# Kernel optimization log

Hardware: AMD Instinct MI355X
Metric: run time of the kernel (lower is better)

## Reference

```python
import jax, jax.numpy as jnp
import numpy as np

N = 100000      # n_nodes
D = 64          # in_features == out_features (elementwise W mul requires equality)
DEG = 16        # avg degree for random edges
H = 2           # n_head
ALPHA = 0.2     # LeakyReLU negative slope


def setup_inputs() -> dict:
    key = jax.random.key(0)
    k1, k2, k3 = jax.random.split(key, 3)
    inputs = jax.random.normal(k1, (N, D), dtype=jnp.float32)
    # random edges + self-loops so every row has at least one edge (nonzero rowsum)
    rnd = jax.random.randint(k2, (2, N * DEG), 0, N)
    self_loops = jnp.tile(jnp.arange(N)[None, :], (2, 1))
    edge_index = jnp.concatenate([self_loops, rnd], axis=1)  # [2, 1.7M]
    # per-head params, matching torch init: W = ones, a ~ U(-stdv, stdv)
    W = jnp.ones((H, D), dtype=jnp.float32)
    stdv = 1.0 / np.sqrt(D * 2)
    a = jax.random.uniform(k3, (H, 2 * D), dtype=jnp.float32, minval=-stdv, maxval=stdv)
    return {"inputs": inputs, "edge_index": edge_index, "W": W, "a": a}


def reference(inputs, edge_index, W, a):
    n = inputs.shape[0]
    row, col = edge_index[0], edge_index[1]

    def head(Wh, ah):
        h = inputs * Wh  # [N, D]
        # a @ [h_src; h_dst] decomposes into per-node dots, then scalar edge gather
        score = (h @ ah[:D])[row] + (h @ ah[D:])[col]          # [E]
        e = jnp.exp(jnp.where(score > 0, score, ALPHA * score))  # exp(leaky_relu)
        rowsum = jax.ops.segment_sum(e, row, num_segments=n)     # [N]
        # sparse.mm(coo(edge, e), inputs): h_prime[i] = sum_j e_ij * inputs[j]
        h_prime = jax.ops.segment_sum(e[:, None] * inputs[col], row, num_segments=n)
        return h_prime / rowsum[:, None]

    outs = jax.vmap(head)(W, a)  # [H, N, D]
    return outs.mean(axis=0)
```

## Files before the change

kernel.cpp:

```cpp
#include <hip/hip_runtime.h>


#define D 64
#define ALPHA 0.2f
#define CAP 96
#define BSHIFT 9
#define BROWS 512
#define MAXBUK 256
#define TILE 2048
#define PACKSHIFT 23
#define COLMASK ((1u << PACKSHIFT) - 1u)

__device__ __forceinline__ unsigned bf16rne(float f) {
    unsigned u = __float_as_uint(f);
    u += 0x7fffu + ((u >> 16) & 1u);
    return u >> 16;
}
__device__ __forceinline__ float lrexp(float sc) {
    return __expf(sc > 0.f ? sc : ALPHA * sc);
}

__global__ __launch_bounds__(256) void k_front(
    const float* __restrict__ x, const float* __restrict__ W,
    const float* __restrict__ a, float4* __restrict__ s,
    unsigned short* __restrict__ xh, const int* __restrict__ row,
    unsigned short* __restrict__ tcnt, int N, int E, int nblkA)
{
    __shared__ int h[MAXBUK];
    if ((int)blockIdx.x < nblkA) {
        int wid  = (blockIdx.x * 256 + threadIdx.x) >> 6;
        int lane = threadIdx.x & 63;
        if (wid >= N) return;
        float v = x[(size_t)wid * D + lane];
        xh[(size_t)wid * D + lane] = (unsigned short)bf16rne(v);
        float h0 = v * W[lane];
        float h1 = v * W[D + lane];
        float t0 = h0 * a[lane];
        float t1 = h0 * a[D + lane];
        float t2 = h1 * a[2 * D + lane];
        float t3 = h1 * a[3 * D + lane];
#pragma unroll
        for (int off = 32; off; off >>= 1) {
            t0 += __shfl_xor(t0, off);
            t1 += __shfl_xor(t1, off);
            t2 += __shfl_xor(t2, off);
            t3 += __shfl_xor(t3, off);
        }
        if (lane == 0) s[wid] = make_float4(t0, t1, t2, t3);
    } else {
        int tile = blockIdx.x - nblkA;
        int t = threadIdx.x, base = tile * TILE;
        int cnt = E - base; if (cnt > TILE) cnt = TILE;
        h[t] = 0;
        __syncthreads();
        for (int i = t; i < cnt; i += 256) atomicAdd(&h[row[base + i] >> BSHIFT], 1);
        __syncthreads();
        tcnt[(size_t)tile * MAXBUK + t] = (unsigned short)h[t];
    }
}

__global__ __launch_bounds__(256) void k_col_scan(
    const unsigned short* __restrict__ tcnt, int* __restrict__ tbase,
    int* __restrict__ bcnt, int NT)
{
    __shared__ int wsum[256];
    int b = blockIdx.x, t = threadIdx.x;
    int t4 = t * 4;
    int v0 = (t4     < NT) ? tcnt[(size_t)(t4    ) * MAXBUK + b] : 0;
    int v1 = (t4 + 1 < NT) ? tcnt[(size_t)(t4 + 1) * MAXBUK + b] : 0;
    int v2 = (t4 + 2 < NT) ? tcnt[(size_t)(t4 + 2) * MAXBUK + b] : 0;
    int v3 = (t4 + 3 < NT) ? tcnt[(size_t)(t4 + 3) * MAXBUK + b] : 0;
    int sv = v0 + v1 + v2 + v3;
    wsum[t] = sv;
    __syncthreads();
    for (int off = 1; off < 256; off <<= 1) {
        int add = (t >= off) ? wsum[t - off] : 0;
        __syncthreads();
        wsum[t] += add;
        __syncthreads();
    }
    int run = wsum[t] - sv;
    if (t4     < NT) { tbase[(size_t)(t4    ) * MAXBUK + b] = run; run += v0; }
    if (t4 + 1 < NT) { tbase[(size_t)(t4 + 1) * MAXBUK + b] = run; run += v1; }
    if (t4 + 2 < NT) { tbase[(size_t)(t4 + 2) * MAXBUK + b] = run; run += v2; }
    if (t4 + 3 < NT) { tbase[(size_t)(t4 + 3) * MAXBUK + b] = run; run += v3; }
    if (t == 255) bcnt[b] = wsum[255];
}

__global__ void k_bucket_scan(const int* __restrict__ bcnt,
                              int* __restrict__ bbase, int nbuk)
{
    __shared__ int sd[MAXBUK];
    int t = threadIdx.x;
    int v = (t < nbuk) ? bcnt[t] : 0;
    sd[t] = v;
    __syncthreads();
    for (int off = 1; off < MAXBUK; off <<= 1) {
        int add = (t >= off) ? sd[t - off] : 0;
        __syncthreads();
        sd[t] += add;
        __syncthreads();
    }
    if (t < nbuk) bbase[t] = sd[t] - v;
    if (t == nbuk - 1) bbase[nbuk] = sd[t];
}

__global__ __launch_bounds__(256) void k_binning(
    const int* __restrict__ row, const int* __restrict__ col,
    const unsigned short* __restrict__ tcnt, const int* __restrict__ bbase,
    const int* __restrict__ tbase, unsigned* __restrict__ ebuf, int E)
{
    __shared__ int lrow[TILE];
    __shared__ int lcol[TILE];
    __shared__ int st[MAXBUK];
    __shared__ int gb[MAXBUK];
    __shared__ int cur[MAXBUK];
    __shared__ int wsum[256];
    int t = threadIdx.x;
    int tile = blockIdx.x;
    int base = tile * TILE;
    int cnt = E - base; if (cnt > TILE) cnt = TILE;

    int h = tcnt[(size_t)tile * MAXBUK + t];
    wsum[t] = h;
    __syncthreads();
    for (int off = 1; off < 256; off <<= 1) {
        int add = (t >= off) ? wsum[t - off] : 0;
        __syncthreads();
        wsum[t] += add;
        __syncthreads();
    }
    int start = wsum[t] - h;
    st[t]  = start;
    cur[t] = start;
    gb[t]  = bbase[t] + tbase[(size_t)tile * MAXBUK + t];
    __syncthreads();

    for (int i = t; i < cnt; i += 256) {
        int r = row[base + i], c = col[base + i];
        int p = atomicAdd(&cur[r >> BSHIFT], 1);
        lrow[p] = r; lcol[p] = c;
    }
    __syncthreads();

    for (int i = t; i < cnt; i += 256) {
        int rr = lrow[i];
        int bb = rr >> BSHIFT;
        ebuf[gb[bb] + (i - st[bb])] =
            ((unsigned)(rr & (BROWS - 1)) << PACKSHIFT) | (unsigned)lcol[i];
    }
}

__global__ __launch_bounds__(1024) void k_rowsort(
    const unsigned* __restrict__ ebuf, const int* __restrict__ bbase,
    int* __restrict__ offsets, int* __restrict__ counts,
    int* __restrict__ scol, int N)
{
    __shared__ int hist[BROWS];
    __shared__ int offs[BROWS];
    __shared__ int wsum[256];
    int b = blockIdx.x, t = threadIdx.x;
    int lo = b << BSHIFT;
    int s0 = bbase[b], s1 = bbase[b + 1];

    if (t < BROWS) hist[t] = 0;
    __syncthreads();
    for (int i = s0 + t; i < s1; i += 1024)
        atomicAdd(&hist[ebuf[i] >> PACKSHIFT], 1);
    __syncthreads();

    int a0 = 0, a1 = 0, sv = 0;
    if (t < 256) { a0 = hist[2 * t]; a1 = hist[2 * t + 1]; sv = a0 + a1; wsum[t] = sv; }
    __syncthreads();
    for (int off = 1; off < 256; off <<= 1) {
        int add = 0;
        if (t < 256 && t >= off) add = wsum[t - off];
        __syncthreads();
        if (t < 256) wsum[t] += add;
        __syncthreads();
    }
    if (t < 256) { int run = wsum[t] - sv; offs[2 * t] = run; offs[2 * t + 1] = run + a0; }
    __syncthreads();

    if (t < BROWS) {
        int rg = lo + t;
        if (rg < N) { offsets[rg] = s0 + offs[t]; counts[rg] = hist[t]; }
    }
    __syncthreads();
    if (t < BROWS) hist[t] = offs[t];
    __syncthreads();

    for (int i = s0 + t; i < s1; i += 1024) {
        unsigned pk = ebuf[i];
        int p = atomicAdd(&hist[pk >> PACKSHIFT], 1);
        scol[s0 + p] = (int)(pk & COLMASK);
    }
}

__global__ __launch_bounds__(256) void k_gather(
    const unsigned* __restrict__ xh2, const float4* __restrict__ s,
    const int* __restrict__ offsets, const int* __restrict__ counts,
    const int* __restrict__ scol, float* __restrict__ out, int N)
{
    __shared__ float  le0[4][CAP];
    __shared__ float  le1[4][CAP];
    __shared__ float2 lpair[4][CAP];
    int w    = threadIdx.x >> 6;
    int lane = threadIdx.x & 63;
    int n    = blockIdx.x * 4 + w;
    bool valid = (n < N);
    int start = 0, cnt = 0;
    float4 srow = make_float4(0.f, 0.f, 0.f, 0.f);
    if (valid) { start = offsets[n]; cnt = counts[n]; srow = s[n]; }

    float sum0 = 0.f, sum1 = 0.f;
    for (int k = lane; k < cnt; k += 64) {
        int c = scol[start + k];
        float4 sc = s[c];
        float e0 = lrexp(srow.x + sc.y);
        float e1 = lrexp(srow.z + sc.w);
        sum0 += e0; sum1 += e1;
        if (k < CAP) { lpair[w][k].x = __int_as_float(c << 5); le0[w][k] = e0; le1[w][k] = e1; }
    }
    int m  = cnt < CAP ? cnt : CAP;
    int mp = (m + 7) & ~7;
    {
        int k = m + lane;
        if (k < mp) { lpair[w][k].x = __int_as_float(0); le0[w][k] = 0.f; le1[w][k] = 0.f; }
    }
#pragma unroll
    for (int off = 32; off; off >>= 1) {
        sum0 += __shfl_xor(sum0, off);
        sum1 += __shfl_xor(sum1, off);
    }
    if (!valid) return;
    float inv0 = 0.5f / sum0, inv1 = 0.5f / sum1;
    for (int k = lane; k < mp; k += 64)
        lpair[w][k].y = inv0 * le0[w][k] + inv1 * le1[w][k];

    int q  = lane >> 4;
    int li = lane & 15;
    float a0 = 0.f, a1 = 0.f, a2 = 0.f, a3 = 0.f;
    for (int k = 0; k < mp; k += 8) {
#pragma unroll
        for (int j = 0; j < 2; j++) {
            int kk = k + 4 * j + q;
            float2 pr = lpair[w][kk];
            unsigned cb = (unsigned)__float_as_int(pr.x);
            uint2 u = *(const uint2*)(xh2 + cb + 2 * li);
            float cf = pr.y;
            a0 += cf * __uint_as_float(u.x << 16);
            a1 += cf * __uint_as_float(u.x & 0xffff0000u);
            a2 += cf * __uint_as_float(u.y << 16);
            a3 += cf * __uint_as_float(u.y & 0xffff0000u);
        }
    }
    for (int kk = CAP + q; kk < cnt; kk += 4) {
        int c = scol[start + kk];
        float4 sc = s[c];
        float cf = inv0 * lrexp(srow.x + sc.y) + inv1 * lrexp(srow.z + sc.w);
        uint2 u = *(const uint2*)(xh2 + ((unsigned)c << 5) + 2 * li);
        a0 += cf * __uint_as_float(u.x << 16);
        a1 += cf * __uint_as_float(u.x & 0xffff0000u);
        a2 += cf * __uint_as_float(u.y << 16);
        a3 += cf * __uint_as_float(u.y & 0xffff0000u);
    }
    a0 += __shfl_xor(a0, 16); a0 += __shfl_xor(a0, 32);
    a1 += __shfl_xor(a1, 16); a1 += __shfl_xor(a1, 32);
    a2 += __shfl_xor(a2, 16); a2 += __shfl_xor(a2, 32);
    a3 += __shfl_xor(a3, 16); a3 += __shfl_xor(a3, 32);
    if (q == 0)
        ((float4*)(out + (size_t)n * D))[li] = make_float4(a0, a1, a2, a3);
}

extern "C" void kernel_launch(void* const* d_in, const int* in_sizes, int n_in,
                              void* d_out, int out_size, void* d_ws, size_t ws_size,
                              hipStream_t stream)
{
    const float* x  = (const float*)d_in[0];
    const int*   ei = (const int*)d_in[1];
    const float* W  = (const float*)d_in[2];
    const float* a  = (const float*)d_in[3];
    float*       out = (float*)d_out;
    int N = in_sizes[0] / D;
    int E = in_sizes[1] / 2;
    const int* row = ei;
    const int* col = ei + E;

    int NBUK = (N + BROWS - 1) >> BSHIFT;
    int NT   = (E + TILE - 1) / TILE;

    uintptr_t wp = (uintptr_t)d_ws;
    auto alloc = [&wp](size_t bytes) -> void* {
        wp = (wp + 255) & ~(uintptr_t)255;
        void* p = (void*)wp;
        wp += bytes;
        return p;
    };
    unsigned short* xh      = (unsigned short*)alloc((size_t)N * D * 2);
    float4*         s       = (float4*)alloc((size_t)N * sizeof(float4));
    int*            offsets = (int*)alloc((size_t)N * sizeof(int));
    int*            counts  = (int*)alloc((size_t)N * sizeof(int));
    int*            scol    = (int*)alloc((size_t)E * sizeof(int));
    unsigned*       ebuf    = (unsigned*)alloc((size_t)E * sizeof(unsigned));
    int*            tbase   = (int*)alloc((size_t)NT * MAXBUK * sizeof(int));
    int*            bcnt    = (int*)alloc(MAXBUK * sizeof(int));
    int*            bbase   = (int*)alloc((MAXBUK + 4) * sizeof(int));
    unsigned short* tcnt    = (unsigned short*)alloc((size_t)NT * MAXBUK * 2);

    int nblkA = (N + 3) / 4;
    k_front<<<nblkA + NT, 256, 0, stream>>>(x, W, a, s, xh, row, tcnt, N, E, nblkA);
    k_col_scan<<<NBUK, 256, 0, stream>>>(tcnt, tbase, bcnt, NT);
    k_bucket_scan<<<1, MAXBUK, 0, stream>>>(bcnt, bbase, NBUK);
    k_binning<<<NT, 256, 0, stream>>>(row, col, tcnt, bbase, tbase, ebuf, E);
    k_rowsort<<<NBUK, 1024, 0, stream>>>(ebuf, bbase, offsets, counts, scol, N);
    k_gather<<<(N + 3) / 4, 256, 0, stream>>>((const unsigned*)xh, s, offsets, counts, scol, out, N);
}
```

Measured before the change: 188.3 us.

## Compute softmax coefficients in row-sort and stream precomputed fp16 weights in gather

Moves per-edge exp(leaky_relu) scoring and row normalisation out of the gather kernel into the row-sort kernel. That kernel now uses 256-row buckets, stages edges in shared memory, and writes pre-shifted column offsets plus fp16 combined coefficients, so the gather becomes a plain weighted sum. It also folds the bucket scan into the binning kernel, removing one launch, and vectorises the front kernel to float4 with four nodes per wave. The trade-offs are extra fp16 rounding of attention weights, larger shared-memory use in row-sort, and a slow fallback path for oversized buckets.

```diff
diff --git a/kernel.cpp b/kernel.cpp
--- a/kernel.cpp
+++ b/kernel.cpp
@@ -1,15 +1,16 @@
 #include <hip/hip_runtime.h>
+#include <hip/hip_fp16.h>
 
 
 #define D 64
 #define ALPHA 0.2f
-#define CAP 96
-#define BSHIFT 9
-#define BROWS 512
-#define MAXBUK 256
+#define BSHIFT 8
+#define BROWS 256
+#define MAXBUK 512
 #define TILE 2048
-#define PACKSHIFT 23
-#define COLMASK ((1u << PACKSHIFT) - 1u)
+#define PK2 17
+#define M17 ((1u << PK2) - 1u)
+#define CAPE 6144
 
 __device__ __forceinline__ unsigned bf16rne(float f) {
     unsigned u = __float_as_uint(f);
@@ -19,52 +20,71 @@
 __device__ __forceinline__ float lrexp(float sc) {
     return __expf(sc > 0.f ? sc : ALPHA * sc);
 }
+__device__ __forceinline__ unsigned packe(float e0, float e1) {
+    __half2 h = __floats2half2_rn(e0, e1);
+    return *reinterpret_cast<unsigned*>(&h);
+}
+__device__ __forceinline__ float2 unpacke(unsigned u) {
+    __half2 h = *reinterpret_cast<__half2*>(&u);
+    return __half22float2(h);
+}
 
 __global__ __launch_bounds__(256) void k_front(
     const float* __restrict__ x, const float* __restrict__ W,
     const float* __restrict__ a, float4* __restrict__ s,
-    unsigned short* __restrict__ xh, const int* __restrict__ row,
+    unsigned* __restrict__ xh2, const int* __restrict__ row,
     unsigned short* __restrict__ tcnt, int N, int E, int nblkA)
 {
     __shared__ int h[MAXBUK];
     if ((int)blockIdx.x < nblkA) {
         int wid  = (blockIdx.x * 256 + threadIdx.x) >> 6;
         int lane = threadIdx.x & 63;
-        if (wid >= N) return;
-        float v = x[(size_t)wid * D + lane];
-        xh[(size_t)wid * D + lane] = (unsigned short)bf16rne(v);
-        float h0 = v * W[lane];
-        float h1 = v * W[D + lane];
-        float t0 = h0 * a[lane];
-        float t1 = h0 * a[D + lane];
-        float t2 = h1 * a[2 * D + lane];
-        float t3 = h1 * a[3 * D + lane];
+        int node = wid * 4 + (lane >> 4);
+        int f4   = lane & 15;
+        if (node >= N) return;
+        const float4* x4 = (const float4*)x;
+        const float4* W4 = (const float4*)W;
+        const float4* A4 = (const float4*)a;
+        float4 v  = x4[(size_t)node * 16 + f4];
+        unsigned u01 = (bf16rne(v.y) << 16) | bf16rne(v.x);
+        unsigned u23 = (bf16rne(v.w) << 16) | bf16rne(v.z);
+        *(uint2*)(xh2 + (size_t)node * 32 + 2 * f4) = make_uint2(u01, u23);
+        float4 w0 = W4[f4], w1 = W4[16 + f4];
+        float4 a0 = A4[f4], a1 = A4[16 + f4], a2 = A4[32 + f4], a3 = A4[48 + f4];
+        float4 h0 = make_float4(v.x * w0.x, v.y * w0.y, v.z * w0.z, v.w * w0.w);
+        float4 h1 = make_float4(v.x * w1.x, v.y * w1.y, v.z * w1.z, v.w * w1.w);
+        float t0 = h0.x * a0.x + h0.y * a0.y + h0.z * a0.z + h0.w * a0.w;
+        float t1 = h0.x * a1.x + h0.y * a1.y + h0.z * a1.z + h0.w * a1.w;
+        float t2 = h1.x * a2.x + h1.y * a2.y + h1.z * a2.z + h1.w * a2.w;
+        float t3 = h1.x * a3.x + h1.y * a3.y + h1.z * a3.z + h1.w * a3.w;
 #pragma unroll
-        for (int off = 32; off; off >>= 1) {
+        for (int off = 1; off < 16; off <<= 1) {
             t0 += __shfl_xor(t0, off);
             t1 += __shfl_xor(t1, off);
             t2 += __shfl_xor(t2, off);
             t3 += __shfl_xor(t3, off);
         }
-        if (lane == 0) s[wid] = make_float4(t0, t1, t2, t3);
+        if (f4 == 0) s[node] = make_float4(t0, t1, t2, t3);
     } else {
         int tile = blockIdx.x - nblkA;
         int t = threadIdx.x, base = tile * TILE;
         int cnt = E - base; if (cnt > TILE) cnt = TILE;
-        h[t] = 0;
+        h[t] = 0; h[t + 256] = 0;
         __syncthreads();
         for (int i = t; i < cnt; i += 256) atomicAdd(&h[row[base + i] >> BSHIFT], 1);
         __syncthreads();
-        tcnt[(size_t)tile * MAXBUK + t] = (unsigned short)h[t];
+        tcnt[(size_t)tile * MAXBUK + t]       = (unsigned short)h[t];
+        tcnt[(size_t)tile * MAXBUK + t + 256] = (unsigned short)h[t + 256];
     }
 }
 
 __global__ __launch_bounds__(256) void k_col_scan(
     const unsigned short* __restrict__ tcnt, int* __restrict__ tbase,
-    int* __restrict__ bcnt, int NT)
-{
+    int* __restrict__ bcnt, int NT, int nbuk)
+{
+    int b = blockIdx.x, t = threadIdx.x;
+    if (b >= nbuk) { if (t == 0) bcnt[b] = 0; return; }
     __shared__ int wsum[256];
-    int b = blockIdx.x, t = threadIdx.x;
     int t4 = t * 4;
     int v0 = (t4     < NT) ? tcnt[(size_t)(t4    ) * MAXBUK + b] : 0;
     int v1 = (t4 + 1 < NT) ? tcnt[(size_t)(t4 + 1) * MAXBUK + b] : 0;
@@ -87,53 +107,56 @@
     if (t == 255) bcnt[b] = wsum[255];
 }
 
-__global__ void k_bucket_scan(const int* __restrict__ bcnt,
-                              int* __restrict__ bbase, int nbuk)
-{
-    __shared__ int sd[MAXBUK];
-    int t = threadIdx.x;
-    int v = (t < nbuk) ? bcnt[t] : 0;
-    sd[t] = v;
-    __syncthreads();
-    for (int off = 1; off < MAXBUK; off <<= 1) {
-        int add = (t >= off) ? sd[t - off] : 0;
-        __syncthreads();
-        sd[t] += add;
-        __syncthreads();
-    }
-    if (t < nbuk) bbase[t] = sd[t] - v;
-    if (t == nbuk - 1) bbase[nbuk] = sd[t];
-}
-
 __global__ __launch_bounds__(256) void k_binning(
     const int* __restrict__ row, const int* __restrict__ col,
-    const unsigned short* __restrict__ tcnt, const int* __restrict__ bbase,
-    const int* __restrict__ tbase, unsigned* __restrict__ ebuf, int E)
+    const unsigned short* __restrict__ tcnt, const int* __restrict__ bcnt,
+    const int* __restrict__ tbase, unsigned* __restrict__ ebuf,
+    int* __restrict__ bbase_g, int E)
 {
     __shared__ int lrow[TILE];
     __shared__ int lcol[TILE];
     __shared__ int st[MAXBUK];
     __shared__ int gb[MAXBUK];
     __shared__ int cur[MAXBUK];
-    __shared__ int wsum[256];
+    __shared__ int w2[256];
     int t = threadIdx.x;
     int tile = blockIdx.x;
     int base = tile * TILE;
     int cnt = E - base; if (cnt > TILE) cnt = TILE;
 
-    int h = tcnt[(size_t)tile * MAXBUK + t];
-    wsum[t] = h;
+    int h0 = tcnt[(size_t)tile * MAXBUK + 2 * t];
+    int h1 = tcnt[(size_t)tile * MAXBUK + 2 * t + 1];
+    int sv = h0 + h1;
+    w2[t] = sv;
     __syncthreads();
     for (int off = 1; off < 256; off <<= 1) {
-        int add = (t >= off) ? wsum[t - off] : 0;
-        __syncthreads();
-        wsum[t] += add;
-        __syncthreads();
-    }
-    int start = wsum[t] - h;
-    st[t]  = start;
-    cur[t] = start;
-    gb[t]  = bbase[t] + tbase[(size_t)tile * MAXBUK + t];
+        int add = (t >= off) ? w2[t - off] : 0;
+        __syncthreads();
+        w2[t] += add;
+        __syncthreads();
+    }
+    int run = w2[t] - sv;
+    st[2 * t] = run;       st[2 * t + 1] = run + h0;
+    cur[2 * t] = run;      cur[2 * t + 1] = run + h0;
+    __syncthreads();
+
+    int b0 = bcnt[2 * t], b1 = bcnt[2 * t + 1];
+    int sb = b0 + b1;
+    w2[t] = sb;
+    __syncthreads();
+    for (int off = 1; off < 256; off <<= 1) {
+        int add = (t >= off) ? w2[t - off] : 0;
+        __syncthreads();
+        w2[t] += add;
+        __syncthreads();
+    }
+    int runb = w2[t] - sb;
+    gb[2 * t]     = runb      + tbase[(size_t)tile * MAXBUK + 2 * t];
+    gb[2 * t + 1] = runb + b0 + tbase[(size_t)tile * MAXBUK + 2 * t + 1];
+    if (tile == 0) {
+        bbase_g[2 * t] = runb; bbase_g[2 * t + 1] = runb + b0;
+        if (t == 255) bbase_g[512] = runb + b0 + b1;
+    }
     __syncthreads();
 
     for (int i = t; i < cnt; i += 256) {
@@ -147,119 +170,126 @@
         int rr = lrow[i];
         int bb = rr >> BSHIFT;
         ebuf[gb[bb] + (i - st[bb])] =
-            ((unsigned)(rr & (BROWS - 1)) << PACKSHIFT) | (unsigned)lcol[i];
+            ((unsigned)(rr & (BROWS - 1)) << PK2) | (unsigned)lcol[i];
     }
 }
 
 __global__ __launch_bounds__(1024) void k_rowsort(
     const unsigned* __restrict__ ebuf, const int* __restrict__ bbase,
-    int* __restrict__ offsets, int* __restrict__ counts,
-    int* __restrict__ scol, int N)
-{
-    __shared__ int hist[BROWS];
-    __shared__ int offs[BROWS];
-    __shared__ int wsum[256];
+    const float4* __restrict__ s, int* __restrict__ offsets,
+    int* __restrict__ counts, unsigned* __restrict__ scol,
+    __half* __restrict__ ecoef, int N)
+{
+    __shared__ unsigned lpk[CAPE];
+    __shared__ unsigned lev[CAPE];
+    __shared__ int   hist[BROWS];
+    __shared__ int   offs[BROWS];
+    __shared__ int   cursor[BROWS];
+    __shared__ float rs0[BROWS], rs1[BROWS];
+    __shared__ float rsx[BROWS], rsz[BROWS];
+    __shared__ int   wsum[256];
     int b = blockIdx.x, t = threadIdx.x;
     int lo = b << BSHIFT;
     int s0 = bbase[b], s1 = bbase[b + 1];
-
-    if (t < BROWS) hist[t] = 0;
-    __syncthreads();
+    int seg = s1 - s0;
+
+    if (t < BROWS) {
+        int g = lo + t;
+        float4 f = (g < N) ? s[g] : make_float4(0.f, 0.f, 0.f, 0.f);
+        rsx[t] = f.x; rsz[t] = f.z;
+        hist[t] = 0; rs0[t] = 0.f; rs1[t] = 0.f;
+    }
+    __syncthreads();
+
     for (int i = s0 + t; i < s1; i += 1024)
-        atomicAdd(&hist[ebuf[i] >> PACKSHIFT], 1);
-    __syncthreads();
-
-    int a0 = 0, a1 = 0, sv = 0;
-    if (t < 256) { a0 = hist[2 * t]; a1 = hist[2 * t + 1]; sv = a0 + a1; wsum[t] = sv; }
+        atomicAdd(&hist[ebuf[i] >> PK2], 1);
+    __syncthreads();
+
+    int a = 0;
+    if (t < BROWS) { a = hist[t]; wsum[t] = a; }
     __syncthreads();
     for (int off = 1; off < 256; off <<= 1) {
         int add = 0;
-        if (t < 256 && t >= off) add = wsum[t - off];
-        __syncthreads();
-        if (t < 256) wsum[t] += add;
-        __syncthreads();
-    }
-    if (t < 256) { int run = wsum[t] - sv; offs[2 * t] = run; offs[2 * t + 1] = run + a0; }
-    __syncthreads();
-
-    if (t < BROWS) {
-        int rg = lo + t;
-        if (rg < N) { offsets[rg] = s0 + offs[t]; counts[rg] = hist[t]; }
-    }
-    __syncthreads();
-    if (t < BROWS) hist[t] = offs[t];
-    __syncthreads();
-
-    for (int i = s0 + t; i < s1; i += 1024) {
-        unsigned pk = ebuf[i];
-        int p = atomicAdd(&hist[pk >> PACKSHIFT], 1);
-        scol[s0 + p] = (int)(pk & COLMASK);
+        if (t < BROWS && t >= off) add = wsum[t - off];
+        __syncthreads();
+        if (t < BROWS) wsum[t] += add;
+        __syncthreads();
+    }
+    if (t < BROWS) { offs[t] = wsum[t] - a; cursor[t] = wsum[t] - a; }
+    __syncthreads();
+
+    if (seg <= CAPE) {
+        for (int i = s0 + t; i < s1; i += 1024) {
+            unsigned pk = ebuf[i];
+            int r = pk >> PK2, c = (int)(pk & M17);
+            float4 sc = s[c];
+            float e0 = lrexp(rsx[r] + sc.y);
+            float e1 = lrexp(rsz[r] + sc.w);
+            atomicAdd(&rs0[r], e0);
+            atomicAdd(&rs1[r], e1);
+            int p = atomicAdd(&cursor[r], 1);
+            lpk[p] = pk; lev[p] = packe(e0, e1);
+        }
+        __syncthreads();
+        if (t < BROWS) {
+            rs0[t] = 0.5f / rs0[t]; rs1[t] = 0.5f / rs1[t];
+            int rg = lo + t;
+            if (rg < N) { offsets[rg] = s0 + offs[t]; counts[rg] = hist[t]; }
+        }
+        __syncthreads();
+        for (int i = t; i < seg; i += 1024) {
+            unsigned pk = lpk[i];
+            int r = pk >> PK2;
+            float2 ef = unpacke(lev[i]);
+            float coef = rs0[r] * ef.x + rs1[r] * ef.y;
+            scol[s0 + i]  = (pk & M17) << 5;
+            ecoef[s0 + i] = __float2half(coef);
+        }
+    } else {
+        for (int i = s0 + t; i < s1; i += 1024) {
+            unsigned pk = ebuf[i];
+            int r = pk >> PK2, c = (int)(pk & M17);
+            float4 sc = s[c];
+            atomicAdd(&rs0[r], lrexp(rsx[r] + sc.y));
+            atomicAdd(&rs1[r], lrexp(rsz[r] + sc.w));
+        }
+        __syncthreads();
+        if (t < BROWS) {
+            rs0[t] = 0.5f / rs0[t]; rs1[t] = 0.5f / rs1[t];
+            int rg = lo + t;
+            if (rg < N) { offsets[rg] = s0 + offs[t]; counts[rg] = hist[t]; }
+        }
+        __syncthreads();
+        for (int i = s0 + t; i < s1; i += 1024) {
+            unsigned pk = ebuf[i];
+            int r = pk >> PK2, c = (int)(pk & M17);
+            float4 sc = s[c];
+            float coef = rs0[r] * lrexp(rsx[r] + sc.y)
+                       + rs1[r] * lrexp(rsz[r] + sc.w);
+            int p = atomicAdd(&cursor[r], 1);
+            scol[s0 + p]  = (unsigned)c << 5;
+            ecoef[s0 + p] = __float2half(coef);
+        }
     }
 }
 
 __global__ __launch_bounds__(256) void k_gather(
-    const unsigned* __restrict__ xh2, const float4* __restrict__ s,
-    const int* __restrict__ offsets, const int* __restrict__ counts,
-    const int* __restrict__ scol, float* __restrict__ out, int N)
-{
-    __shared__ float  le0[4][CAP];
-    __shared__ float  le1[4][CAP];
-    __shared__ float2 lpair[4][CAP];
+    const unsigned* __restrict__ xh2, const int* __restrict__ offsets,
+    const int* __restrict__ counts, const unsigned* __restrict__ scol,
+    const __half* __restrict__ ecoef, float* __restrict__ out, int N)
+{
     int w    = threadIdx.x >> 6;
     int lane = threadIdx.x & 63;
     int n    = blockIdx.x * 4 + w;
-    bool valid = (n < N);
-    int start = 0, cnt = 0;
-    float4 srow = make_float4(0.f, 0.f, 0.f, 0.f);
-    if (valid) { start = offsets[n]; cnt = counts[n]; srow = s[n]; }
-
-    float sum0 = 0.f, sum1 = 0.f;
-    for (int k = lane; k < cnt; k += 64) {
-        int c = scol[start + k];
-        float4 sc = s[c];
-        float e0 = lrexp(srow.x + sc.y);
-        float e1 = lrexp(srow.z + sc.w);
-        sum0 += e0; sum1 += e1;
-        if (k < CAP) { lpair[w][k].x = __int_as_float(c << 5); le0[w][k] = e0; le1[w][k] = e1; }
-    }
-    int m  = cnt < CAP ? cnt : CAP;
-    int mp = (m + 7) & ~7;
-    {
-        int k = m + lane;
-        if (k < mp) { lpair[w][k].x = __int_as_float(0); le0[w][k] = 0.f; le1[w][k] = 0.f; }
-    }
-#pragma unroll
-    for (int off = 32; off; off >>= 1) {
-        sum0 += __shfl_xor(sum0, off);
-        sum1 += __shfl_xor(sum1, off);
-    }
-    if (!valid) return;
-    float inv0 = 0.5f / sum0, inv1 = 0.5f / sum1;
-    for (int k = lane; k < mp; k += 64)
-        lpair[w][k].y = inv0 * le0[w][k] + inv1 * le1[w][k];
-
+    if (n >= N) return;
+    int start = offsets[n], cnt = counts[n];
     int q  = lane >> 4;
     int li = lane & 15;
     float a0 = 0.f, a1 = 0.f, a2 = 0.f, a3 = 0.f;
-    for (int k = 0; k < mp; k += 8) {
-#pragma unroll
-        for (int j = 0; j < 2; j++) {
-            int kk = k + 4 * j + q;
-            float2 pr = lpair[w][kk];
-            unsigned cb = (unsigned)__float_as_int(pr.x);
-            uint2 u = *(const uint2*)(xh2 + cb + 2 * li);
-            float cf = pr.y;
-            a0 += cf * __uint_as_float(u.x << 16);
-            a1 += cf * __uint_as_float(u.x & 0xffff0000u);
-            a2 += cf * __uint_as_float(u.y << 16);
-            a3 += cf * __uint_as_float(u.y & 0xffff0000u);
-        }
-    }
-    for (int kk = CAP + q; kk < cnt; kk += 4) {
-        int c = scol[start + kk];
-        float4 sc = s[c];
-        float cf = inv0 * lrexp(srow.x + sc.y) + inv1 * lrexp(srow.z + sc.w);
-        uint2 u = *(const uint2*)(xh2 + ((unsigned)c << 5) + 2 * li);
+    for (int kk = q; kk < cnt; kk += 4) {
+        unsigned cb = scol[start + kk];
+        float cf = __half2float(ecoef[start + kk]);
+        uint2 u = *(const uint2*)(xh2 + cb + 2 * li);
         a0 += cf * __uint_as_float(u.x << 16);
         a1 += cf * __uint_as_float(u.x & 0xffff0000u);
         a2 += cf * __uint_as_float(u.y << 16);
@@ -297,22 +327,22 @@
         wp += bytes;
         return p;
     };
-    unsigned short* xh      = (unsigned short*)alloc((size_t)N * D * 2);
+    unsigned*       xh2     = (unsigned*)alloc((size_t)N * 32 * 4);
     float4*         s       = (float4*)alloc((size_t)N * sizeof(float4));
     int*            offsets = (int*)alloc((size_t)N * sizeof(int));
     int*            counts  = (int*)alloc((size_t)N * sizeof(int));
-    int*            scol    = (int*)alloc((size_t)E * sizeof(int));
+    unsigned*       scol    = (unsigned*)alloc((size_t)E * sizeof(unsigned));
     unsigned*       ebuf    = (unsigned*)alloc((size_t)E * sizeof(unsigned));
+    __half*         ecoef   = (__half*)alloc((size_t)E * sizeof(__half));
     int*            tbase   = (int*)alloc((size_t)NT * MAXBUK * sizeof(int));
     int*            bcnt    = (int*)alloc(MAXBUK * sizeof(int));
     int*            bbase   = (int*)alloc((MAXBUK + 4) * sizeof(int));
     unsigned short* tcnt    = (unsigned short*)alloc((size_t)NT * MAXBUK * 2);
 
-    int nblkA = (N + 3) / 4;
-    k_front<<<nblkA + NT, 256, 0, stream>>>(x, W, a, s, xh, row, tcnt, N, E, nblkA);
-    k_col_scan<<<NBUK, 256, 0, stream>>>(tcnt, tbase, bcnt, NT);
-    k_bucket_scan<<<1, MAXBUK, 0, stream>>>(bcnt, bbase, NBUK);
-    k_binning<<<NT, 256, 0, stream>>>(row, col, tcnt, bbase, tbase, ebuf, E);
-    k_rowsort<<<NBUK, 1024, 0, stream>>>(ebuf, bbase, offsets, counts, scol, N);
-    k_gather<<<(N + 3) / 4, 256, 0, stream>>>((const unsigned*)xh, s, offsets, counts, scol, out, N);
-}
+    int nblkA = (N + 15) / 16;
+    k_front<<<nblkA + NT, 256, 0, stream>>>(x, W, a, s, xh2, row, tcnt, N, E, nblkA);
+    k_col_scan<<<MAXBUK, 256, 0, stream>>>(tcnt, tbase, bcnt, NT, NBUK);
+    k_binning<<<NT, 256, 0, stream>>>(row, col, tcnt, bcnt, tbase, ebuf, bbase, E);
+    k_rowsort<<<NBUK, 1024, 0, stream>>>(ebuf, bbase, s, offsets, counts, scol, ecoef, N);
+    k_gather<<<(N + 3) / 4, 256, 0, stream>>>(xh2, offsets, counts, scol, ecoef, out, N);
+}
```

Measured after the change: 199.2 us. 5.8% more time.
